# Kernel tuning notes

Measured on AMD Instinct MI355X. Metric: run time of the kernel, lower is better.

## Reference

```python
import jax, jax.numpy as jnp
import numpy as np

B, T, D = 4, 1024, 256
H, DK, C = 8, 32, 16  # n_heads, d_key, pos-encoder hidden units
DV = D // H
NEG = -1e15
EPS_SM = 1e-5
EPS_LN = 1e-5
SLOPE = 0.01  # LeakyReLU default


def setup_inputs() -> dict:
    key = jax.random.key(0)
    ks = jax.random.split(key, 16)
    s = 0.05
    x = jax.random.normal(ks[0], (B, T, D), jnp.float32)
    src_mask = jax.random.randint(ks[1], (B, T, T), 0, 2).astype(bool)
    rel_dists = jax.random.uniform(ks[2], (B, 1, T, T), jnp.float32)
    Wq = jax.random.normal(ks[3], (H, DK, D), jnp.float32) * s
    Wk = jax.random.normal(ks[4], (H, DK, D), jnp.float32) * s
    Wv = jax.random.normal(ks[5], (H, DV, D), jnp.float32) * s
    pw1 = jax.random.normal(ks[6], (H, C), jnp.float32) * s
    pb1 = jax.random.normal(ks[7], (H, C), jnp.float32) * s
    pw2 = jax.random.normal(ks[8], (H, C), jnp.float32) * s
    pb2 = jax.random.normal(ks[9], (H,), jnp.float32) * s
    Wo = jax.random.normal(ks[10], (D, D), jnp.float32) * s
    bo = jax.random.normal(ks[11], (D,), jnp.float32) * s
    Wf = jax.random.normal(ks[12], (D, D), jnp.float32) * s
    bf = jax.random.normal(ks[13], (D,), jnp.float32) * s
    g1 = jnp.ones((D,), jnp.float32)
    beta1 = jnp.zeros((D,), jnp.float32)
    g2 = jnp.ones((D,), jnp.float32)
    beta2 = jnp.zeros((D,), jnp.float32)
    return dict(x=x, src_mask=src_mask, rel_dists=rel_dists, Wq=Wq, Wk=Wk, Wv=Wv,
                pw1=pw1, pb1=pb1, pw2=pw2, pb2=pb2, Wo=Wo, bo=bo, Wf=Wf, bf=bf,
                g1=g1, beta1=beta1, g2=g2, beta2=beta2)


def _l2norm(v):
    # F.normalize(p=2, dim=-1): v / max(||v||, 1e-12)
    n = jnp.sqrt(jnp.sum(v * v, axis=-1, keepdims=True))
    return v / jnp.maximum(n, 1e-12)


def _lrelu(h):
    return jnp.where(h >= 0, h, SLOPE * h)


def _pos_bias(d, pw1, pb1, pw2, pb2):
    # d: [B,T,T]; per-head 1x1-conv MLP applied elementwise.
    # Loop over the tiny channel dim (16) to avoid a [B,H,T,T,C] intermediate.
    bias = jnp.broadcast_to(pb2[None, :, None, None], (d.shape[0], pw1.shape[0], d.shape[1], d.shape[2]))
    for c in range(pw1.shape[1]):
        h = d[:, None] * pw1[None, :, c, None, None] + pb1[None, :, c, None, None]
        bias = bias + pw2[None, :, c, None, None] * _lrelu(h)
    return bias  # [B,H,T,T]


def _layer_norm(v, g, b):
    mu = jnp.mean(v, axis=-1, keepdims=True)
    var = jnp.mean((v - mu) ** 2, axis=-1, keepdims=True)
    return (v - mu) * jax.lax.rsqrt(var + EPS_LN) * g + b


def reference(x, src_mask, rel_dists, Wq, Wk, Wv, pw1, pb1, pw2, pb2,
              Wo, bo, Wf, bf, g1, beta1, g2, beta2):
    # cosine-normalized multi-head attention (all heads batched)
    q = _l2norm(jnp.einsum('btd,hkd->bhtk', x, Wq))
    k = _l2norm(jnp.einsum('bsd,hkd->bhsk', x, Wk))
    v = jnp.einsum('bsd,hvd->bhsv', x, Wv)
    logits = jnp.einsum('bhtk,bhsk->bhts', q, k)
    logits = logits - _pos_bias(rel_dists[:, 0], pw1, pb1, pw2, pb2)
    logits = jnp.where(src_mask[:, None], NEG, logits)
    # custom softmax: exp / (sum + 1e-5) (handles all-padded rows)
    z = jnp.exp(logits)
    attn = z / (jnp.sum(z, axis=-1, keepdims=True) + EPS_SM)
    heads = jnp.einsum('bhts,bhsv->bhtv', attn, v)
    y = heads.transpose(0, 2, 1, 3).reshape(x.shape[0], x.shape[1], -1)  # concat heads
    y = y @ Wo.T + bo
    # residual + LN + FFN (dropout is identity in eval mode)
    zz = _layer_norm(x + y, g1, beta1)
    z_ff = _lrelu(zz @ Wf.T + bf)
    return _layer_norm(zz + z_ff, g2, beta2)
```

## Files before the change

### kernel.cpp

```cpp
#include <hip/hip_runtime.h>
#include <math.h>

#define Bc 4
#define Tc 1024
#define Dc 256
#define Hc 8
#define Cc 16
#define LUTN 256

typedef __attribute__((ext_vector_type(8))) short short8;
typedef __attribute__((ext_vector_type(4))) float f32x4;

__device__ __forceinline__ unsigned bf16u(float x) {
    unsigned u = __float_as_uint(x);
    return (u + 0x7FFFu + ((u >> 16) & 1u)) >> 16;
}
__device__ __forceinline__ unsigned pk2(float lo, float hi) {
    return bf16u(lo) | (bf16u(hi) << 16);
}
__device__ __forceinline__ unsigned pk2t(float lo, float hi) {
    return __builtin_amdgcn_perm(__float_as_uint(hi), __float_as_uint(lo), 0x07060302u);
}
__device__ __forceinline__ float upk(unsigned v) { return __uint_as_float(v << 16); }
__device__ __forceinline__ float upkh(unsigned v) { return __uint_as_float(v & 0xffff0000u); }

__global__ __launch_bounds__(256) void cast_all(
    const float* __restrict__ x,
    const float* __restrict__ Wq, const float* __restrict__ Wk,
    const float* __restrict__ Wv, const float* __restrict__ Wo,
    const float* __restrict__ Wf,
    const float* __restrict__ pw1, const float* __restrict__ pb1,
    const float* __restrict__ pw2, const float* __restrict__ pb2,
    ushort* __restrict__ Xc, ushort* __restrict__ Wqkvc,
    ushort* __restrict__ Woc, ushort* __restrict__ Wfc,
    ushort* __restrict__ LUTb)
{
    if (blockIdx.x == 1344) {
        const int bin = threadIdx.x;
        const float d0 = bin * (1.f / LUTN), d1 = (bin + 1) * (1.f / LUTN);
        for (int h = 0; h < Hc; ++h) {
            float y0 = pb2[h], y1 = pb2[h];
#pragma unroll
            for (int c = 0; c < Cc; ++c) {
                float w1 = pw1[h * Cc + c], b1 = pb1[h * Cc + c], w2 = pw2[h * Cc + c];
                float h0 = fmaf(w1, d0, b1), h1 = fmaf(w1, d1, b1);
                y0 = fmaf(w2, h0 >= 0.f ? h0 : 0.01f * h0, y0);
                y1 = fmaf(w2, h1 >= 0.f ? h1 : 0.01f * h1, y1);
            }
            float a = (y1 - y0) * (float)LUTN;
            float b = y0 - a * d0;
            LUTb[(h >> 2) * 2048 + bin * 8 + (h & 3) * 2]     = (ushort)bf16u(a);
            LUTb[(h >> 2) * 2048 + bin * 8 + (h & 3) * 2 + 1] = (ushort)bf16u(b);
        }
        return;
    }
    const int e = (blockIdx.x * 256 + threadIdx.x) * 4;
    const float* src; ushort* dst; int off;
    if (e < 1048576)      { src = x;  dst = Xc;             off = e; }
    else if (e < 1114112) { src = Wq; dst = Wqkvc;          off = e - 1048576; }
    else if (e < 1179648) { src = Wk; dst = Wqkvc + 65536;  off = e - 1114112; }
    else if (e < 1245184) { src = Wv; dst = Wqkvc + 131072; off = e - 1179648; }
    else if (e < 1310720) { src = Wo; dst = Woc;            off = e - 1245184; }
    else                  { src = Wf; dst = Wfc;            off = e - 1310720; }
    float4 v = *(const float4*)(src + off);
    uint2 p; p.x = pk2(v.x, v.y); p.y = pk2(v.z, v.w);
    *(uint2*)(dst + off) = p;
}

__global__ __launch_bounds__(256) void qkv_direct(
    const ushort* __restrict__ Xc, const ushort* __restrict__ Wqkv,
    ushort* __restrict__ Qb, ushort* __restrict__ Kb, ushort* __restrict__ Vt)
{
    const int tid = threadIdx.x;
    const int w = tid >> 6;
    const int l = tid & 63;
    const int u = l & 15, g = l >> 4;
    const int rbase = blockIdx.x * 16;
    const int cb = (blockIdx.y * 4 + w) * 64;

    f32x4 acc[4];
#pragma unroll
    for (int nt = 0; nt < 4; ++nt) acc[nt] = (f32x4){0.f, 0.f, 0.f, 0.f};

    const ushort* arow = Xc + (size_t)(rbase + u) * 256 + g * 8;
#pragma unroll 2
    for (int k0 = 0; k0 < 256; k0 += 32) {
        short8 af = *(const short8*)(arow + k0);
#pragma unroll
        for (int nt = 0; nt < 4; ++nt) {
            short8 bfr = *(const short8*)(Wqkv + (size_t)(cb + nt * 16 + u) * 256 + k0 + g * 8);
            acc[nt] = __builtin_amdgcn_mfma_f32_16x16x32_bf16(af, bfr, acc[nt], 0, 0, 0);
        }
    }

    const int mat = cb >> 8;
    const int fcb = cb & 255;
    if (mat < 2) {
        ushort* Out = (mat == 0) ? Qb : Kb;
#pragma unroll
        for (int hp = 0; hp < 2; ++hp) {
            const int head = (fcb >> 5) + hp;
#pragma unroll
            for (int reg = 0; reg < 4; ++reg) {
                float ss = acc[2 * hp][reg] * acc[2 * hp][reg]
                         + acc[2 * hp + 1][reg] * acc[2 * hp + 1][reg];
                ss += __shfl_xor(ss, 1, 64);
                ss += __shfl_xor(ss, 2, 64);
                ss += __shfl_xor(ss, 4, 64);
                ss += __shfl_xor(ss, 8, 64);
                float scn = 1.f / fmaxf(sqrtf(ss), 1e-12f);
                const int t = rbase + 4 * g + reg;
                const int bb = t >> 10, tt = t & 1023;
                const size_t base = ((size_t)(bb * 8 + head) * Tc + tt) * 32;
                Out[base + u]      = (ushort)bf16u(acc[2 * hp][reg] * scn);
                Out[base + 16 + u] = (ushort)bf16u(acc[2 * hp + 1][reg] * scn);
            }
        }
    } else {
#pragma unroll
        for (int nt = 0; nt < 4; ++nt) {
            const int head = (fcb >> 5) + (nt >> 1);
            const int vt = nt & 1;
#pragma unroll
            for (int reg = 0; reg < 4; ++reg) {
                const int s = rbase + 4 * g + reg;
                const int bb = s >> 10, ss = s & 1023;
                const int bh = bb * 8 + head;
                Vt[(((size_t)bh * 32 + (ss >> 5)) * 2 + vt) * 512 + u * 32 + (ss & 31)] =
                    (ushort)bf16u(acc[nt][reg]);
            }
        }
    }
}

__global__ __launch_bounds__(256) void attn_mfma(
    const ushort* __restrict__ Qb, const ushort* __restrict__ Kb,
    const ushort* __restrict__ Vt,
    const float* __restrict__ rel, const int* __restrict__ msk,
    const ushort* __restrict__ LUTb,
    ushort* __restrict__ Yb)
{
    const int tid = threadIdx.x;
    const int w = tid >> 6;
    const int l = tid & 63;
    const int u = l & 15;
    const int g = l >> 4;
    const int t0 = blockIdx.x * 16;
    const int b = blockIdx.y;
    const int hg = blockIdx.z;

    __shared__ __align__(16) ushort lut_s[2048];
    __shared__ __align__(16) unsigned plds[4 * 320];
    __shared__ __align__(16) ushort comb[4 * 16 * 136];
    __shared__ float rs_s[4 * 64];

    *(uint4*)(lut_s + tid * 8) = *(const uint4*)(LUTb + hg * 2048 + tid * 8);

    const int bh0 = b * 8 + hg * 4;
    short8 qf[4];
#pragma unroll
    for (int hi = 0; hi < 4; ++hi)
        qf[hi] = *(const short8*)(Qb + (((size_t)(bh0 + hi) * Tc + t0 + u) * 32 + g * 8));

    const short8 ones = (short8){0x3F80, 0x3F80, 0x3F80, 0x3F80,
                                 0x3F80, 0x3F80, 0x3F80, 0x3F80};

    f32x4 oacc[4][2];
    f32x4 rsacc[4];
#pragma unroll
    for (int hi = 0; hi < 4; ++hi) {
        oacc[hi][0] = (f32x4){0.f, 0.f, 0.f, 0.f};
        oacc[hi][1] = (f32x4){0.f, 0.f, 0.f, 0.f};
        rsacc[hi]   = (f32x4){0.f, 0.f, 0.f, 0.f};
    }

    unsigned* pwb = plds + w * 320;
    const size_t dbase = (size_t)b * Tc * Tc;

    __syncthreads();

    const int s_begin = w * 256;
    for (int sc = s_begin; sc < s_begin + 256; sc += 32) {
        float dA[4], dB[4];
#pragma unroll
        for (int reg = 0; reg < 4; ++reg) {
            const int t = t0 + 4 * g + reg;
            const size_t off = dbase + (size_t)t * Tc + sc + 2 * u;
            float2 d2 = *(const float2*)(rel + off);
            int2 m2 = *(const int2*)(msk + off);
            dA[reg] = m2.x ? -1.f : d2.x;
            dB[reg] = m2.y ? -1.f : d2.y;
        }
        float biasA[4][4], biasB[4][4];
#pragma unroll
        for (int reg = 0; reg < 4; ++reg) {
            int iA = (int)(dA[reg] * (float)LUTN);
            int iB = (int)(dB[reg] * (float)LUTN);
            iA = iA < 0 ? 0 : (iA > LUTN - 1 ? LUTN - 1 : iA);
            iB = iB < 0 ? 0 : (iB > LUTN - 1 ? LUTN - 1 : iB);
            uint4 wA = *(const uint4*)(lut_s + iA * 8);
            uint4 wB = *(const uint4*)(lut_s + iB * 8);
            biasA[reg][0] = fmaf(upk(wA.x), dA[reg], upkh(wA.x));
            biasA[reg][1] = fmaf(upk(wA.y), dA[reg], upkh(wA.y));
            biasA[reg][2] = fmaf(upk(wA.z), dA[reg], upkh(wA.z));
            biasA[reg][3] = fmaf(upk(wA.w), dA[reg], upkh(wA.w));
            biasB[reg][0] = fmaf(upk(wB.x), dB[reg], upkh(wB.x));
            biasB[reg][1] = fmaf(upk(wB.y), dB[reg], upkh(wB.y));
            biasB[reg][2] = fmaf(upk(wB.z), dB[reg], upkh(wB.z));
            biasB[reg][3] = fmaf(upk(wB.w), dB[reg], upkh(wB.w));
        }
        const size_t vtile = ((size_t)0 + (sc >> 5)) * 1024;
#pragma unroll
        for (int hi = 0; hi < 4; ++hi) {
            const size_t kb = ((size_t)(bh0 + hi) * Tc + sc + 2 * u) * 32 + g * 8;
            short8 kfA = *(const short8*)(Kb + kb);
            short8 kfB = *(const short8*)(Kb + kb + 32);
            const f32x4 z4 = (f32x4){0.f, 0.f, 0.f, 0.f};
            f32x4 sA = __builtin_amdgcn_mfma_f32_16x16x32_bf16(qf[hi], kfA, z4, 0, 0, 0);
            f32x4 sB = __builtin_amdgcn_mfma_f32_16x16x32_bf16(qf[hi], kfB, z4, 0, 0, 0);
#pragma unroll
            for (int reg = 0; reg < 4; ++reg) {
                float zA = (dA[reg] < 0.f) ? 0.f : __expf(sA[reg] - biasA[reg][hi]);
                float zB = (dB[reg] < 0.f) ? 0.f : __expf(sB[reg] - biasB[reg][hi]);
                pwb[(4 * g + reg) * 20 + u] = pk2t(zA, zB);
            }
            short8 pf = *(const short8*)((const char*)pwb + u * 80 + g * 16);
            const ushort* vb = Vt + ((size_t)(bh0 + hi) * 32 + (sc >> 5)) * 1024;
            short8 vf0 = *(const short8*)(vb + u * 32 + g * 8);
            short8 vf1 = *(const short8*)(vb + 512 + u * 32 + g * 8);
            oacc[hi][0] = __builtin_amdgcn_mfma_f32_16x16x32_bf16(pf, vf0, oacc[hi][0], 0, 0, 0);
            oacc[hi][1] = __builtin_amdgcn_mfma_f32_16x16x32_bf16(pf, vf1, oacc[hi][1], 0, 0, 0);
            rsacc[hi]   = __builtin_amdgcn_mfma_f32_16x16x32_bf16(pf, ones, rsacc[hi], 0, 0, 0);
        }
        (void)vtile;
    }

#pragma unroll
    for (int hi = 0; hi < 4; ++hi)
        if (u == 0) {
#pragma unroll
            for (int reg = 0; reg < 4; ++reg)
                rs_s[(w * 4 + hi) * 16 + 4 * g + reg] = rsacc[hi][reg];
        }
#pragma unroll
    for (int hi = 0; hi < 4; ++hi)
#pragma unroll
        for (int vt = 0; vt < 2; ++vt)
#pragma unroll
            for (int reg = 0; reg < 4; ++reg)
                comb[w * 2176 + (4 * g + reg) * 136 + hi * 32 + vt * 16 + u] =
                    (ushort)pk2t(0.f, oacc[hi][vt][reg]) >> 0 ? (ushort)(__float_as_uint(oacc[hi][vt][reg]) >> 16) : (ushort)(__float_as_uint(oacc[hi][vt][reg]) >> 16);
    __syncthreads();

    const int tl = tid >> 4;
    const int f0 = (tid & 15) * 8;
    const int hl = f0 >> 5;
    float rstot = rs_s[(0 + hl) * 16 + tl] + rs_s[(4 + hl) * 16 + tl]
                + rs_s[(8 + hl) * 16 + tl] + rs_s[(12 + hl) * 16 + tl];
    float inv = 1.f / (rstot + 1e-5f);
    float o[8];
#pragma unroll
    for (int k = 0; k < 8; ++k) o[k] = 0.f;
#pragma unroll
    for (int ww = 0; ww < 4; ++ww) {
        uint4 pv = *(const uint4*)&comb[ww * 2176 + tl * 136 + f0];
        o[0] += upk(pv.x); o[1] += upkh(pv.x);
        o[2] += upk(pv.y); o[3] += upkh(pv.y);
        o[4] += upk(pv.z); o[5] += upkh(pv.z);
        o[6] += upk(pv.w); o[7] += upkh(pv.w);
    }
    uint4 pw;
    pw.x = pk2(o[0] * inv, o[1] * inv); pw.y = pk2(o[2] * inv, o[3] * inv);
    pw.z = pk2(o[4] * inv, o[5] * inv); pw.w = pk2(o[6] * inv, o[7] * inv);
    *(uint4*)(Yb + ((size_t)b * Tc + t0 + tl) * Dc + hg * 128 + f0) = pw;
}

__global__ __launch_bounds__(256) void gemm_ln(
    const ushort* __restrict__ A, const ushort* __restrict__ W,
    const float* __restrict__ bias,
    const float* __restrict__ resF, const ushort* __restrict__ resB,
    const float* __restrict__ gam, const float* __restrict__ bet,
    float* __restrict__ outF, ushort* __restrict__ outB, int act)
{
    const int tid = threadIdx.x;
    const int w = tid >> 6;
    const int l = tid & 63;
    const int u = l & 15, g = l >> 4;
    const int rbase = blockIdx.x * 16;

    __shared__ float red1[64], red2[64];

    f32x4 acc[4];
#pragma unroll
    for (int nt = 0; nt < 4; ++nt) acc[nt] = (f32x4){0.f, 0.f, 0.f, 0.f};

    const ushort* arow = A + (size_t)(rbase + u) * 256 + g * 8;
#pragma unroll 2
    for (int k0 = 0; k0 < 256; k0 += 32) {
        short8 af = *(const short8*)(arow + k0);
#pragma unroll
        for (int nt = 0; nt < 4; ++nt) {
            short8 bfr = *(const short8*)(W + (size_t)(w * 64 + nt * 16 + u) * 256 + k0 + g * 8);
            acc[nt] = __builtin_amdgcn_mfma_f32_16x16x32_bf16(af, bfr, acc[nt], 0, 0, 0);
        }
    }

    float bv[4];
#pragma unroll
    for (int nt = 0; nt < 4; ++nt) bv[nt] = bias[w * 64 + nt * 16 + u];

    float sv[4][4];
#pragma unroll
    for (int reg = 0; reg < 4; ++reg) {
        const int row = rbase + 4 * g + reg;
        float s1 = 0.f, s2 = 0.f;
#pragma unroll
        for (int nt = 0; nt < 4; ++nt) {
            const int col = w * 64 + nt * 16 + u;
            float v = acc[nt][reg] + bv[nt];
            if (act) v = v >= 0.f ? v : 0.01f * v;
            float res = resF ? resF[(size_t)row * 256 + col]
                             : upk((unsigned)resB[(size_t)row * 256 + col]);
            float s = v + res;
            sv[reg][nt] = s;
            s1 += s;
            s2 = fmaf(s, s, s2);
        }
        s1 += __shfl_xor(s1, 1, 64); s2 += __shfl_xor(s2, 1, 64);
        s1 += __shfl_xor(s1, 2, 64); s2 += __shfl_xor(s2, 2, 64);
        s1 += __shfl_xor(s1, 4, 64); s2 += __shfl_xor(s2, 4, 64);
        s1 += __shfl_xor(s1, 8, 64); s2 += __shfl_xor(s2, 8, 64);
        if (u == 0) { red1[w * 16 + 4 * g + reg] = s1; red2[w * 16 + 4 * g + reg] = s2; }
    }
    __syncthreads();

    float gv[4], btv[4];
#pragma unroll
    for (int nt = 0; nt < 4; ++nt) {
        gv[nt]  = gam[w * 64 + nt * 16 + u];
        btv[nt] = bet[w * 64 + nt * 16 + u];
    }
#pragma unroll
    for (int reg = 0; reg < 4; ++reg) {
        const int row = rbase + 4 * g + reg;
        const int rl = 4 * g + reg;
        float S1 = red1[rl] + red1[16 + rl] + red1[32 + rl] + red1[48 + rl];
        float S2 = red2[rl] + red2[16 + rl] + red2[32 + rl] + red2[48 + rl];
        float mu = S1 * (1.f / 256.f);
        float var = S2 * (1.f / 256.f) - mu * mu;
        float rsig = rsqrtf(var + 1e-5f);
#pragma unroll
        for (int nt = 0; nt < 4; ++nt) {
            const int col = w * 64 + nt * 16 + u;
            float o = (sv[reg][nt] - mu) * rsig * gv[nt] + btv[nt];
            if (outF) outF[(size_t)row * 256 + col] = o;
            else      outB[(size_t)row * 256 + col] = (ushort)bf16u(o);
        }
    }
}

extern "C" void kernel_launch(void* const* d_in, const int* in_sizes, int n_in,
                              void* d_out, int out_size, void* d_ws, size_t ws_size,
                              hipStream_t stream) {
    const float* x    = (const float*)d_in[0];
    const int*   mask = (const int*)d_in[1];
    const float* rel  = (const float*)d_in[2];
    const float* Wq   = (const float*)d_in[3];
    const float* Wk   = (const float*)d_in[4];
    const float* Wv   = (const float*)d_in[5];
    const float* pw1  = (const float*)d_in[6];
    const float* pb1  = (const float*)d_in[7];
    const float* pw2  = (const float*)d_in[8];
    const float* pb2  = (const float*)d_in[9];
    const float* Wo   = (const float*)d_in[10];
    const float* bo   = (const float*)d_in[11];
    const float* Wf   = (const float*)d_in[12];
    const float* bf   = (const float*)d_in[13];
    const float* g1   = (const float*)d_in[14];
    const float* be1  = (const float*)d_in[15];
    const float* g2   = (const float*)d_in[16];
    const float* be2  = (const float*)d_in[17];
    float* out = (float*)d_out;

    char* wsb = (char*)d_ws;
    ushort* Xc    = (ushort*)(wsb);
    ushort* Qb    = (ushort*)(wsb + (size_t)( 2 << 20));
    ushort* Kb    = (ushort*)(wsb + (size_t)( 4 << 20));
    ushort* Vt    = (ushort*)(wsb + (size_t)( 6 << 20));
    ushort* Yb    = (ushort*)(wsb + (size_t)( 8 << 20));
    ushort* Wqkvc = (ushort*)(wsb + (size_t)(10 << 20));
    ushort* Woc   = (ushort*)(wsb + (size_t)(10 << 20) + (512 << 10));
    ushort* Wfc   = (ushort*)(wsb + (size_t)(10 << 20) + (768 << 10));
    ushort* LUTb  = (ushort*)(wsb + (size_t)(11 << 20));
    ushort* ZZb   = (ushort*)(wsb + (size_t)(12 << 20));

    cast_all<<<1345, 256, 0, stream>>>(x, Wq, Wk, Wv, Wo, Wf,
                                       pw1, pb1, pw2, pb2,
                                       Xc, Wqkvc, Woc, Wfc, LUTb);
    qkv_direct<<<dim3(256, 3), 256, 0, stream>>>(Xc, Wqkvc, Qb, Kb, Vt);
    attn_mfma<<<dim3(64, 4, 2), 256, 0, stream>>>(Qb, Kb, Vt, rel, mask, LUTb, Yb);
    gemm_ln<<<256, 256, 0, stream>>>(Yb, Woc, bo, x, nullptr, g1, be1,
                                     nullptr, ZZb, 0);
    gemm_ln<<<256, 256, 0, stream>>>(ZZb, Wfc, bf, nullptr, ZZb, g2, be2,
                                     out, nullptr, 1);
}
```

Before: 175.1 us.

## Precompact rel/mask into bf16 distance map and split attention per head pair

```diff
diff --git a/kernel.cpp b/kernel.cpp
--- a/kernel.cpp
+++ b/kernel.cpp
@@ -1,7 +1,6 @@
 #include <hip/hip_runtime.h>
 #include <math.h>
 
-#define Bc 4
 #define Tc 1024
 #define Dc 256
 #define Hc 8
@@ -25,18 +24,20 @@
 __device__ __forceinline__ float upkh(unsigned v) { return __uint_as_float(v & 0xffff0000u); }
 
 __global__ __launch_bounds__(256) void cast_all(
-    const float* __restrict__ x,
+    const float* __restrict__ rel, const int* __restrict__ msk,
     const float* __restrict__ Wq, const float* __restrict__ Wk,
     const float* __restrict__ Wv, const float* __restrict__ Wo,
     const float* __restrict__ Wf,
     const float* __restrict__ pw1, const float* __restrict__ pb1,
     const float* __restrict__ pw2, const float* __restrict__ pb2,
-    ushort* __restrict__ Xc, ushort* __restrict__ Wqkvc,
-    ushort* __restrict__ Woc, ushort* __restrict__ Wfc,
-    ushort* __restrict__ LUTb)
+    ushort* __restrict__ Wqkvc, ushort* __restrict__ Woc,
+    ushort* __restrict__ Wfc, ushort* __restrict__ LUTb,
+    ushort* __restrict__ Dm)
 {
-    if (blockIdx.x == 1344) {
-        const int bin = threadIdx.x;
+    const int bid = blockIdx.x;
+    const int tid = threadIdx.x;
+    if (bid == 320) {
+        const int bin = tid;
         const float d0 = bin * (1.f / LUTN), d1 = (bin + 1) * (1.f / LUTN);
         for (int h = 0; h < Hc; ++h) {
             float y0 = pb2[h], y1 = pb2[h];
@@ -49,26 +50,35 @@
             }
             float a = (y1 - y0) * (float)LUTN;
             float b = y0 - a * d0;
-            LUTb[(h >> 2) * 2048 + bin * 8 + (h & 3) * 2]     = (ushort)bf16u(a);
-            LUTb[(h >> 2) * 2048 + bin * 8 + (h & 3) * 2 + 1] = (ushort)bf16u(b);
+            LUTb[(h >> 1) * 1024 + bin * 4 + (h & 1) * 2]     = (ushort)bf16u(a);
+            LUTb[(h >> 1) * 1024 + bin * 4 + (h & 1) * 2 + 1] = (ushort)bf16u(b);
         }
         return;
     }
-    const int e = (blockIdx.x * 256 + threadIdx.x) * 4;
-    const float* src; ushort* dst; int off;
-    if (e < 1048576)      { src = x;  dst = Xc;             off = e; }
-    else if (e < 1114112) { src = Wq; dst = Wqkvc;          off = e - 1048576; }
-    else if (e < 1179648) { src = Wk; dst = Wqkvc + 65536;  off = e - 1114112; }
-    else if (e < 1245184) { src = Wv; dst = Wqkvc + 131072; off = e - 1179648; }
-    else if (e < 1310720) { src = Wo; dst = Woc;            off = e - 1245184; }
-    else                  { src = Wf; dst = Wfc;            off = e - 1310720; }
-    float4 v = *(const float4*)(src + off);
-    uint2 p; p.x = pk2(v.x, v.y); p.y = pk2(v.z, v.w);
-    *(uint2*)(dst + off) = p;
+    if (bid < 320) {
+        const int e = bid * 1024 + tid * 4;
+        const float* src; ushort* dst; int off;
+        if      (e <  65536) { src = Wq; dst = Wqkvc;          off = e; }
+        else if (e < 131072) { src = Wk; dst = Wqkvc + 65536;  off = e - 65536; }
+        else if (e < 196608) { src = Wv; dst = Wqkvc + 131072; off = e - 131072; }
+        else if (e < 262144) { src = Wo; dst = Woc;            off = e - 196608; }
+        else                 { src = Wf; dst = Wfc;            off = e - 262144; }
+        float4 v = *(const float4*)(src + off);
+        uint2 p; p.x = pk2(v.x, v.y); p.y = pk2(v.z, v.w);
+        *(uint2*)(dst + off) = p;
+        return;
+    }
+    const int idx = (bid - 321) * 1024 + tid * 4;
+    float4 d4 = *(const float4*)(rel + idx);
+    int4   m4 = *(const int4*)(msk + idx);
+    uint2 p;
+    p.x = (m4.x ? 0xBF80u : bf16u(d4.x)) | ((m4.y ? 0xBF80u : bf16u(d4.y)) << 16);
+    p.y = (m4.z ? 0xBF80u : bf16u(d4.z)) | ((m4.w ? 0xBF80u : bf16u(d4.w)) << 16);
+    *(uint2*)(Dm + idx) = p;
 }
 
 __global__ __launch_bounds__(256) void qkv_direct(
-    const ushort* __restrict__ Xc, const ushort* __restrict__ Wqkv,
+    const float* __restrict__ x, const ushort* __restrict__ Wqkv,
     ushort* __restrict__ Qb, ushort* __restrict__ Kb, ushort* __restrict__ Vt)
 {
     const int tid = threadIdx.x;
@@ -82,14 +92,18 @@
 #pragma unroll
     for (int nt = 0; nt < 4; ++nt) acc[nt] = (f32x4){0.f, 0.f, 0.f, 0.f};
 
-    const ushort* arow = Xc + (size_t)(rbase + u) * 256 + g * 8;
+    const float* arow = x + (size_t)(rbase + u) * 256 + g * 8;
 #pragma unroll 2
     for (int k0 = 0; k0 < 256; k0 += 32) {
-        short8 af = *(const short8*)(arow + k0);
+        float4 a0 = *(const float4*)(arow + k0);
+        float4 a1 = *(const float4*)(arow + k0 + 4);
+        union { short8 s; unsigned wds[4]; } A;
+        A.wds[0] = pk2(a0.x, a0.y); A.wds[1] = pk2(a0.z, a0.w);
+        A.wds[2] = pk2(a1.x, a1.y); A.wds[3] = pk2(a1.z, a1.w);
 #pragma unroll
         for (int nt = 0; nt < 4; ++nt) {
             short8 bfr = *(const short8*)(Wqkv + (size_t)(cb + nt * 16 + u) * 256 + k0 + g * 8);
-            acc[nt] = __builtin_amdgcn_mfma_f32_16x16x32_bf16(af, bfr, acc[nt], 0, 0, 0);
+            acc[nt] = __builtin_amdgcn_mfma_f32_16x16x32_bf16(A.s, bfr, acc[nt], 0, 0, 0);
         }
     }
 
@@ -135,8 +149,7 @@
 
 __global__ __launch_bounds__(256) void attn_mfma(
     const ushort* __restrict__ Qb, const ushort* __restrict__ Kb,
-    const ushort* __restrict__ Vt,
-    const float* __restrict__ rel, const int* __restrict__ msk,
+    const ushort* __restrict__ Vt, const ushort* __restrict__ Dm,
     const ushort* __restrict__ LUTb,
     ushort* __restrict__ Yb)
 {
@@ -149,26 +162,27 @@
     const int b = blockIdx.y;
     const int hg = blockIdx.z;
 
-    __shared__ __align__(16) ushort lut_s[2048];
+    __shared__ __align__(16) ushort lut_s[1024];
     __shared__ __align__(16) unsigned plds[4 * 320];
-    __shared__ __align__(16) ushort comb[4 * 16 * 136];
-    __shared__ float rs_s[4 * 64];
-
-    *(uint4*)(lut_s + tid * 8) = *(const uint4*)(LUTb + hg * 2048 + tid * 8);
-
-    const int bh0 = b * 8 + hg * 4;
-    short8 qf[4];
-#pragma unroll
-    for (int hi = 0; hi < 4; ++hi)
+    __shared__ __align__(16) ushort comb[4 * 16 * 72];
+    __shared__ float rs_s[8 * 16];
+
+    if (tid < 128)
+        *(uint4*)(lut_s + tid * 8) = *(const uint4*)(LUTb + hg * 1024 + tid * 8);
+
+    const int bh0 = b * 8 + hg * 2;
+    short8 qf[2];
+#pragma unroll
+    for (int hi = 0; hi < 2; ++hi)
         qf[hi] = *(const short8*)(Qb + (((size_t)(bh0 + hi) * Tc + t0 + u) * 32 + g * 8));
 
     const short8 ones = (short8){0x3F80, 0x3F80, 0x3F80, 0x3F80,
                                  0x3F80, 0x3F80, 0x3F80, 0x3F80};
 
-    f32x4 oacc[4][2];
-    f32x4 rsacc[4];
-#pragma unroll
-    for (int hi = 0; hi < 4; ++hi) {
+    f32x4 oacc[2][2];
+    f32x4 rsacc[2];
+#pragma unroll
+    for (int hi = 0; hi < 2; ++hi) {
         oacc[hi][0] = (f32x4){0.f, 0.f, 0.f, 0.f};
         oacc[hi][1] = (f32x4){0.f, 0.f, 0.f, 0.f};
         rsacc[hi]   = (f32x4){0.f, 0.f, 0.f, 0.f};
@@ -180,38 +194,45 @@
     __syncthreads();
 
     const int s_begin = w * 256;
+    unsigned dmv[4];
+#pragma unroll
+    for (int reg = 0; reg < 4; ++reg) {
+        const int t = t0 + 4 * g + reg;
+        dmv[reg] = *(const unsigned*)(Dm + dbase + (size_t)t * Tc + s_begin + 2 * u);
+    }
+
     for (int sc = s_begin; sc < s_begin + 256; sc += 32) {
+        unsigned dmn[4] = {0, 0, 0, 0};
+        const int nx = sc + 32;
+        if (nx < s_begin + 256) {
+#pragma unroll
+            for (int reg = 0; reg < 4; ++reg) {
+                const int t = t0 + 4 * g + reg;
+                dmn[reg] = *(const unsigned*)(Dm + dbase + (size_t)t * Tc + nx + 2 * u);
+            }
+        }
         float dA[4], dB[4];
 #pragma unroll
         for (int reg = 0; reg < 4; ++reg) {
-            const int t = t0 + 4 * g + reg;
-            const size_t off = dbase + (size_t)t * Tc + sc + 2 * u;
-            float2 d2 = *(const float2*)(rel + off);
-            int2 m2 = *(const int2*)(msk + off);
-            dA[reg] = m2.x ? -1.f : d2.x;
-            dB[reg] = m2.y ? -1.f : d2.y;
-        }
-        float biasA[4][4], biasB[4][4];
+            dA[reg] = upk(dmv[reg]);
+            dB[reg] = upkh(dmv[reg]);
+        }
+        float biasA[4][2], biasB[4][2];
 #pragma unroll
         for (int reg = 0; reg < 4; ++reg) {
             int iA = (int)(dA[reg] * (float)LUTN);
             int iB = (int)(dB[reg] * (float)LUTN);
             iA = iA < 0 ? 0 : (iA > LUTN - 1 ? LUTN - 1 : iA);
             iB = iB < 0 ? 0 : (iB > LUTN - 1 ? LUTN - 1 : iB);
-            uint4 wA = *(const uint4*)(lut_s + iA * 8);
-            uint4 wB = *(const uint4*)(lut_s + iB * 8);
+            uint2 wA = *(const uint2*)(lut_s + iA * 4);
+            uint2 wB = *(const uint2*)(lut_s + iB * 4);
             biasA[reg][0] = fmaf(upk(wA.x), dA[reg], upkh(wA.x));
             biasA[reg][1] = fmaf(upk(wA.y), dA[reg], upkh(wA.y));
-            biasA[reg][2] = fmaf(upk(wA.z), dA[reg], upkh(wA.z));
-            biasA[reg][3] = fmaf(upk(wA.w), dA[reg], upkh(wA.w));
             biasB[reg][0] = fmaf(upk(wB.x), dB[reg], upkh(wB.x));
             biasB[reg][1] = fmaf(upk(wB.y), dB[reg], upkh(wB.y));
-            biasB[reg][2] = fmaf(upk(wB.z), dB[reg], upkh(wB.z));
-            biasB[reg][3] = fmaf(upk(wB.w), dB[reg], upkh(wB.w));
-        }
-        const size_t vtile = ((size_t)0 + (sc >> 5)) * 1024;
-#pragma unroll
-        for (int hi = 0; hi < 4; ++hi) {
+        }
+#pragma unroll
+        for (int hi = 0; hi < 2; ++hi) {
             const size_t kb = ((size_t)(bh0 + hi) * Tc + sc + 2 * u) * 32 + g * 8;
             short8 kfA = *(const short8*)(Kb + kb);
             short8 kfB = *(const short8*)(Kb + kb + 32);
@@ -232,47 +253,50 @@
             oacc[hi][1] = __builtin_amdgcn_mfma_f32_16x16x32_bf16(pf, vf1, oacc[hi][1], 0, 0, 0);
             rsacc[hi]   = __builtin_amdgcn_mfma_f32_16x16x32_bf16(pf, ones, rsacc[hi], 0, 0, 0);
         }
-        (void)vtile;
-    }
-
-#pragma unroll
-    for (int hi = 0; hi < 4; ++hi)
+#pragma unroll
+        for (int reg = 0; reg < 4; ++reg) dmv[reg] = dmn[reg];
+    }
+
+#pragma unroll
+    for (int hi = 0; hi < 2; ++hi)
         if (u == 0) {
 #pragma unroll
             for (int reg = 0; reg < 4; ++reg)
-                rs_s[(w * 4 + hi) * 16 + 4 * g + reg] = rsacc[hi][reg];
-        }
-#pragma unroll
-    for (int hi = 0; hi < 4; ++hi)
+                rs_s[(w * 2 + hi) * 16 + 4 * g + reg] = rsacc[hi][reg];
+        }
+#pragma unroll
+    for (int hi = 0; hi < 2; ++hi)
 #pragma unroll
         for (int vt = 0; vt < 2; ++vt)
 #pragma unroll
             for (int reg = 0; reg < 4; ++reg)
-                comb[w * 2176 + (4 * g + reg) * 136 + hi * 32 + vt * 16 + u] =
-                    (ushort)pk2t(0.f, oacc[hi][vt][reg]) >> 0 ? (ushort)(__float_as_uint(oacc[hi][vt][reg]) >> 16) : (ushort)(__float_as_uint(oacc[hi][vt][reg]) >> 16);
+                comb[w * 1152 + (4 * g + reg) * 72 + hi * 32 + vt * 16 + u] =
+                    (ushort)(__float_as_uint(oacc[hi][vt][reg]) >> 16);
     __syncthreads();
 
-    const int tl = tid >> 4;
-    const int f0 = (tid & 15) * 8;
-    const int hl = f0 >> 5;
-    float rstot = rs_s[(0 + hl) * 16 + tl] + rs_s[(4 + hl) * 16 + tl]
-                + rs_s[(8 + hl) * 16 + tl] + rs_s[(12 + hl) * 16 + tl];
-    float inv = 1.f / (rstot + 1e-5f);
-    float o[8];
-#pragma unroll
-    for (int k = 0; k < 8; ++k) o[k] = 0.f;
-#pragma unroll
-    for (int ww = 0; ww < 4; ++ww) {
-        uint4 pv = *(const uint4*)&comb[ww * 2176 + tl * 136 + f0];
-        o[0] += upk(pv.x); o[1] += upkh(pv.x);
-        o[2] += upk(pv.y); o[3] += upkh(pv.y);
-        o[4] += upk(pv.z); o[5] += upkh(pv.z);
-        o[6] += upk(pv.w); o[7] += upkh(pv.w);
-    }
-    uint4 pw;
-    pw.x = pk2(o[0] * inv, o[1] * inv); pw.y = pk2(o[2] * inv, o[3] * inv);
-    pw.z = pk2(o[4] * inv, o[5] * inv); pw.w = pk2(o[6] * inv, o[7] * inv);
-    *(uint4*)(Yb + ((size_t)b * Tc + t0 + tl) * Dc + hg * 128 + f0) = pw;
+    if (tid < 128) {
+        const int tl = tid >> 3;
+        const int f0 = (tid & 7) * 8;
+        const int hl = f0 >> 5;
+        float rstot = rs_s[hl * 16 + tl] + rs_s[(2 + hl) * 16 + tl]
+                    + rs_s[(4 + hl) * 16 + tl] + rs_s[(6 + hl) * 16 + tl];
+        float inv = 1.f / (rstot + 1e-5f);
+        float o[8];
+#pragma unroll
+        for (int k = 0; k < 8; ++k) o[k] = 0.f;
+#pragma unroll
+        for (int ww = 0; ww < 4; ++ww) {
+            uint4 pv = *(const uint4*)&comb[ww * 1152 + tl * 72 + f0];
+            o[0] += upk(pv.x); o[1] += upkh(pv.x);
+            o[2] += upk(pv.y); o[3] += upkh(pv.y);
+            o[4] += upk(pv.z); o[5] += upkh(pv.z);
+            o[6] += upk(pv.w); o[7] += upkh(pv.w);
+        }
+        uint4 pwv;
+        pwv.x = pk2(o[0] * inv, o[1] * inv); pwv.y = pk2(o[2] * inv, o[3] * inv);
+        pwv.z = pk2(o[4] * inv, o[5] * inv); pwv.w = pk2(o[6] * inv, o[7] * inv);
+        *(uint4*)(Yb + ((size_t)b * Tc + t0 + tl) * Dc + hg * 64 + f0) = pwv;
+    }
 }
 
 __global__ __launch_bounds__(256) void gemm_ln(
@@ -383,22 +407,22 @@
     float* out = (float*)d_out;
 
     char* wsb = (char*)d_ws;
-    ushort* Xc    = (ushort*)(wsb);
-    ushort* Qb    = (ushort*)(wsb + (size_t)( 2 << 20));
-    ushort* Kb    = (ushort*)(wsb + (size_t)( 4 << 20));
-    ushort* Vt    = (ushort*)(wsb + (size_t)( 6 << 20));
-    ushort* Yb    = (ushort*)(wsb + (size_t)( 8 << 20));
-    ushort* Wqkvc = (ushort*)(wsb + (size_t)(10 << 20));
-    ushort* Woc   = (ushort*)(wsb + (size_t)(10 << 20) + (512 << 10));
-    ushort* Wfc   = (ushort*)(wsb + (size_t)(10 << 20) + (768 << 10));
-    ushort* LUTb  = (ushort*)(wsb + (size_t)(11 << 20));
-    ushort* ZZb   = (ushort*)(wsb + (size_t)(12 << 20));
-
-    cast_all<<<1345, 256, 0, stream>>>(x, Wq, Wk, Wv, Wo, Wf,
+    ushort* Qb    = (ushort*)(wsb);
+    ushort* Kb    = (ushort*)(wsb + (size_t)( 2 << 20));
+    ushort* Vt    = (ushort*)(wsb + (size_t)( 4 << 20));
+    ushort* Yb    = (ushort*)(wsb + (size_t)( 6 << 20));
+    ushort* Wqkvc = (ushort*)(wsb + (size_t)( 8 << 20));
+    ushort* Woc   = (ushort*)(wsb + (size_t)( 8 << 20) + (512 << 10));
+    ushort* Wfc   = (ushort*)(wsb + (size_t)( 8 << 20) + (768 << 10));
+    ushort* LUTb  = (ushort*)(wsb + (size_t)( 9 << 20));
+    ushort* ZZb   = (ushort*)(wsb + (size_t)(10 << 20));
+    ushort* Dm    = (ushort*)(wsb + (size_t)(12 << 20));
+
+    cast_all<<<4417, 256, 0, stream>>>(rel, mask, Wq, Wk, Wv, Wo, Wf,
                                        pw1, pb1, pw2, pb2,
-                                       Xc, Wqkvc, Woc, Wfc, LUTb);
-    qkv_direct<<<dim3(256, 3), 256, 0, stream>>>(Xc, Wqkvc, Qb, Kb, Vt);
-    attn_mfma<<<dim3(64, 4, 2), 256, 0, stream>>>(Qb, Kb, Vt, rel, mask, LUTb, Yb);
+                                       Wqkvc, Woc, Wfc, LUTb, Dm);
+    qkv_direct<<<dim3(256, 3), 256, 0, stream>>>(x, Wqkvc, Qb, Kb, Vt);
+    attn_mfma<<<dim3(64, 4, 4), 256, 0, stream>>>(Qb, Kb, Vt, Dm, LUTb, Yb);
     gemm_ln<<<256, 256, 0, stream>>>(Yb, Woc, bo, x, nullptr, g1, be1,
                                      nullptr, ZZb, 0);
     gemm_ln<<<256, 256, 0, stream>>>(ZZb, Wfc, bf, nullptr, ZZb, g2, be2,
```

Result: no change. 176.3 us (+0.7%).
